# Kernel tuning notes

Measured on AMD Instinct MI355X. Metric: run time of the kernel, lower is better.

Reference implementation:

```python
import jax, jax.numpy as jnp
import numpy as np

B, N, M, C, H, NNZ = 64, 2048, 2048, 64, 128, 32768


def setup_inputs() -> dict:
    key = jax.random.key(0)
    ks = jax.random.split(key, 7)
    x = jax.random.normal(ks[0], (B * N, H), dtype=jnp.float32)
    batch = jnp.repeat(jnp.arange(B, dtype=jnp.int32), N)  # sorted graph ids
    d_rows = jax.random.randint(ks[1], (B, NNZ), 0, M, dtype=jnp.int32)
    d_cols = jax.random.randint(ks[2], (B, NNZ), 0, N, dtype=jnp.int32)
    d_vals = jax.random.normal(ks[3], (B, NNZ), dtype=jnp.float32) * (1.0 / np.sqrt(16.0))
    d_index = jax.random.randint(ks[4], (B, M), 0, C, dtype=jnp.int32)
    w_scale = 1.0 / np.sqrt(3 * H)
    Wq = jax.random.normal(ks[5], (3 * H, H), dtype=jnp.float32) * w_scale
    Wk = jax.random.normal(ks[6], (3 * H, H), dtype=jnp.float32) * w_scale
    Wv = jax.random.normal(jax.random.fold_in(key, 7), (3 * H, H), dtype=jnp.float32) * w_scale
    return {"x": x, "batch": batch, "batch_size": B, "d_rows": d_rows,
            "d_cols": d_cols, "d_vals": d_vals, "d_index": d_index,
            "Wq": Wq, "Wk": Wk, "Wv": Wv}


def _per_graph(xg, rows, cols, vals, idx, Wq, Wk, Wv):
    # spmm: coefs[r] = sum_e vals[e] * xg[cols[e]] for rows[e] == r  -> [M, H]
    coefs = jax.ops.segment_sum(vals[:, None] * xg[cols], rows, num_segments=M)
    # three segment poolings over cluster index -> each [C, H]
    s = jax.ops.segment_sum(coefs, idx, num_segments=C)
    cnt = jax.ops.segment_sum(jnp.ones((M,), coefs.dtype), idx, num_segments=C)
    mean = s / jnp.maximum(cnt, 1.0)[:, None]
    mx = jax.ops.segment_max(coefs, idx, num_segments=C)
    x_dec = jnp.concatenate([mean, mx, s], axis=1)  # [C, 3H]
    # small self-attention over clusters (linear layers without bias)
    Q = x_dec @ Wq
    K = x_dec @ Wk
    V = x_dec @ Wv
    dist = jax.nn.softmax((Q @ K.T) * (1.0 / np.sqrt(H)), axis=-1)
    return (dist @ V).reshape(-1)  # [C*H]


def reference(x, batch, batch_size, d_rows, d_cols, d_vals, d_index, Wq, Wk, Wv):
    # nodes are sorted by graph with equal graph size N, so x[batch==i] == xb[i]
    xb = x.reshape(batch_size, N, H)
    out = jax.vmap(_per_graph, in_axes=(0, 0, 0, 0, 0, None, None, None))(
        xb, d_rows, d_cols, d_vals, d_index, Wq, Wk, Wv)
    return out  # [B, C*H] == torch.vstack of per-graph flattened attentions
```

## Files before the change

### kernel.cpp

```cpp
#include <hip/hip_runtime.h>
#include <hip/hip_fp16.h>

#define BG 64
#define NN 2048
#define MM 2048
#define CC 64
#define HH 128
#define NNZE 32768
#define TH 384

typedef float f4v __attribute__((ext_vector_type(4)));
typedef __attribute__((ext_vector_type(8))) short bf16x8;
typedef __attribute__((ext_vector_type(4))) float f32x4;
typedef unsigned short u16;

static __device__ __forceinline__ u16 bf16rne(float f) {
    uint u = __float_as_uint(f);
    uint r = u + 0x7FFFu + ((u >> 16) & 1u);
    return (u16)(r >> 16);
}
static __device__ __forceinline__ float bf16tof(u16 h) {
    return __uint_as_float(((uint)h) << 16);
}

__global__ __launch_bounds__(1024) void prep_all_kernel(
    const int* __restrict__ d_rows, const int* __restrict__ d_cols,
    const float* __restrict__ d_vals, const int* __restrict__ d_index,
    const float* __restrict__ x,
    const float* __restrict__ Wq, const float* __restrict__ Wk,
    const float* __restrict__ Wv,
    uint* __restrict__ xh, u16* __restrict__ WhT, u16* __restrict__ WlT,
    int* __restrict__ cnt_clu_g, int* __restrict__ off_clu_g,
    int* __restrict__ row_edge_off_g, int2* __restrict__ epack) {
    __shared__ int cnt_row_s[MM];
    __shared__ int off_row_s[MM];
    __shared__ int fill_s[MM];
    __shared__ int rlist_s[MM];
    __shared__ int cnt_clu_s[CC], off_clu_s[CC], fill_clu_s[CC];
    __shared__ int wsum[16];
    int g = blockIdx.x, t = threadIdx.x;
    int lane = t & 63, w = t >> 6;

    cnt_row_s[t] = 0;
    cnt_row_s[t + 1024] = 0;
    fill_s[t] = 0;
    fill_s[t + 1024] = 0;
    if (t < CC) {
        cnt_clu_s[t] = 0;
        fill_clu_s[t] = 0;
    }
    int idx0 = d_index[(g << 11) + t];
    int idx1 = d_index[(g << 11) + t + 1024];
    __syncthreads();

    const int4* rows4 = (const int4*)(d_rows + ((size_t)g << 15));
#pragma unroll
    for (int it = 0; it < 8; it++) {
        int4 r = rows4[it * 1024 + t];
        atomicAdd(&cnt_row_s[r.x], 1);
        atomicAdd(&cnt_row_s[r.y], 1);
        atomicAdd(&cnt_row_s[r.z], 1);
        atomicAdd(&cnt_row_s[r.w], 1);
    }
    atomicAdd(&cnt_clu_s[idx0], 1);
    atomicAdd(&cnt_clu_s[idx1], 1);
    __syncthreads();

    if (t < CC) {
        int v = cnt_clu_s[t];
        int incl = v;
#pragma unroll
        for (int d = 1; d < 64; d <<= 1) {
            int u = __shfl_up(incl, d);
            if (t >= d) incl += u;
        }
        off_clu_s[t] = incl - v;
        cnt_clu_g[(g << 6) + t] = v;
        off_clu_g[(g << 6) + t] = incl - v;
    }
    __syncthreads();

    {
        int s0 = atomicAdd(&fill_clu_s[idx0], 1);
        rlist_s[off_clu_s[idx0] + s0] = t;
        int s1 = atomicAdd(&fill_clu_s[idx1], 1);
        rlist_s[off_clu_s[idx1] + s1] = t + 1024;
    }
    __syncthreads();

    int r0 = rlist_s[2 * t], r1 = rlist_s[2 * t + 1];
    int c0 = cnt_row_s[r0], c1 = cnt_row_s[r1];
    int s = c0 + c1;
    int incl = s;
#pragma unroll
    for (int d = 1; d < 64; d <<= 1) {
        int u = __shfl_up(incl, d);
        if (lane >= d) incl += u;
    }
    if (lane == 63) wsum[w] = incl;
    __syncthreads();
    if (t < 16) {
        int v = wsum[t], iv = v;
#pragma unroll
        for (int d = 1; d < 16; d <<= 1) {
            int u = __shfl_up(iv, d);
            if (t >= d) iv += u;
        }
        wsum[t] = iv - v;
    }
    __syncthreads();
    {
        int base = wsum[w] + incl - s;
        int* reo = row_edge_off_g + g * (MM + 1);
        reo[2 * t] = base;
        reo[2 * t + 1] = base + c0;
        off_row_s[r0] = base;
        off_row_s[r1] = base + c0;
        if (t == 0) reo[MM] = NNZE;
    }
    __syncthreads();

    const int4* cols4 = (const int4*)(d_cols + ((size_t)g << 15));
    const f4v* vals4 = (const f4v*)(d_vals + ((size_t)g << 15));
    int2* epg = epack + ((size_t)g << 15);
#pragma unroll
    for (int it = 0; it < 8; it++) {
        int4 r = rows4[it * 1024 + t];
        int4 c = cols4[it * 1024 + t];
        f4v v = vals4[it * 1024 + t];
        {
            int sl = atomicAdd(&fill_s[r.x], 1);
            int flag = (sl == cnt_row_s[r.x] - 1) ? (int)0x80000000 : 0;
            epg[off_row_s[r.x] + sl] = make_int2(c.x | flag, __float_as_int(v.x));
        }
        {
            int sl = atomicAdd(&fill_s[r.y], 1);
            int flag = (sl == cnt_row_s[r.y] - 1) ? (int)0x80000000 : 0;
            epg[off_row_s[r.y] + sl] = make_int2(c.y | flag, __float_as_int(v.y));
        }
        {
            int sl = atomicAdd(&fill_s[r.z], 1);
            int flag = (sl == cnt_row_s[r.z] - 1) ? (int)0x80000000 : 0;
            epg[off_row_s[r.z] + sl] = make_int2(c.z | flag, __float_as_int(v.z));
        }
        {
            int sl = atomicAdd(&fill_s[r.w], 1);
            int flag = (sl == cnt_row_s[r.w] - 1) ? (int)0x80000000 : 0;
            epg[off_row_s[r.w] + sl] = make_int2(c.w | flag, __float_as_int(v.w));
        }
    }

    {
        const f4v* x4 = (const f4v*)(x + ((size_t)g << 18));
        uint4* xh4 = (uint4*)(xh + ((size_t)g << 17));
#pragma unroll 4
        for (int it = 0; it < 32; it++) {
            int gi = it * 1024 + t;
            f4v a = __builtin_nontemporal_load(&x4[2 * gi]);
            f4v b = __builtin_nontemporal_load(&x4[2 * gi + 1]);
            __half2 h0 = __float22half2_rn(make_float2(a.x, a.y));
            __half2 h1 = __float22half2_rn(make_float2(a.z, a.w));
            __half2 h2 = __float22half2_rn(make_float2(b.x, b.y));
            __half2 h3 = __float22half2_rn(make_float2(b.z, b.w));
            uint4 o;
            o.x = *(uint*)&h0;
            o.y = *(uint*)&h1;
            o.z = *(uint*)&h2;
            o.w = *(uint*)&h3;
            xh4[gi] = o;
        }
    }
    for (int i = t; i < 2304; i += 1024) {
        int id = g * 2304 + i;
        int wsel = id / 49152;
        int r = id - wsel * 49152;
        const float* Ws = (wsel == 0) ? Wq : (wsel == 1) ? Wk : Wv;
        float v = Ws[r];
        int k = r >> 7, n = r & 127;
        u16 hi = bf16rne(v);
        u16 lo = bf16rne(v - bf16tof(hi));
        WhT[wsel * 49152 + n * 384 + k] = hi;
        WlT[wsel * 49152 + n * 384 + k] = lo;
    }
}

__global__ __launch_bounds__(64) void spmm_pool_kernel(const uint* __restrict__ xh,
                                                       const int* __restrict__ cnt_clu,
                                                       const int* __restrict__ off_clu,
                                                       const int* __restrict__ row_edge_off,
                                                       const int2* __restrict__ epack,
                                                       u16* __restrict__ xdh,
                                                       u16* __restrict__ xdl) {
    int bid = blockIdx.x;
    int l = bid >> 3;
    int g = ((bid & 7) << 3) + (l >> 6);
    int c = l & 63;
    int h = threadIdx.x;
    int gc = (g << 6) + c;
    int rcnt = cnt_clu[gc];
    int j0 = off_clu[gc];
    const int* reo = row_edge_off + g * (MM + 1) + j0;
    int ebase = reo[0];
    int etot = reo[rcnt] - ebase;
    const long long* ep = (const long long*)(epack + ((size_t)g << 15)) + ebase;
    const uint* xg = xh + ((size_t)g << 17);
    float2 coef = make_float2(0.f, 0.f), sum = make_float2(0.f, 0.f);
    float2 mx = make_float2(-__builtin_inff(), -__builtin_inff());
    int e = 0;
    for (; e + 16 <= etot; e += 16) {
        long long q[16];
#pragma unroll
        for (int k = 0; k < 16; k++) q[k] = __builtin_nontemporal_load(&ep[e + k]);
        uint xv[16];
#pragma unroll
        for (int k = 0; k < 16; k++)
            xv[k] = xg[(((uint)(int)q[k] & 0x7FFFFFFFu) << 6) + h];
#pragma unroll
        for (int k = 0; k < 16; k++) {
            float v = __int_as_float((int)(q[k] >> 32));
            float2 f = __half22float2(*(__half2*)&xv[k]);
            coef.x = fmaf(v, f.x, coef.x);
            coef.y = fmaf(v, f.y, coef.y);
            if ((int)q[k] < 0) {
                sum.x += coef.x; sum.y += coef.y;
                mx.x = fmaxf(mx.x, coef.x); mx.y = fmaxf(mx.y, coef.y);
                coef.x = 0.f; coef.y = 0.f;
            }
        }
    }
    for (; e < etot; e++) {
        long long q = ep[e];
        uint xv = xg[(((uint)(int)q & 0x7FFFFFFFu) << 6) + h];
        float v = __int_as_float((int)(q >> 32));
        float2 f = __half22float2(*(__half2*)&xv);
        coef.x = fmaf(v, f.x, coef.x);
        coef.y = fmaf(v, f.y, coef.y);
        if ((int)q < 0) {
            sum.x += coef.x; sum.y += coef.y;
            mx.x = fmaxf(mx.x, coef.x); mx.y = fmaxf(mx.y, coef.y);
            coef.x = 0.f; coef.y = 0.f;
        }
    }
    int az = 0;
    for (int j = h; j < rcnt; j += 64) az |= (reo[j + 1] == reo[j]);
    if (__ballot(az) != 0ULL) {
        mx.x = fmaxf(mx.x, 0.f);
        mx.y = fmaxf(mx.y, 0.f);
    }
    float inv = 1.f / (float)(rcnt > 0 ? rcnt : 1);
    uint* oh = (uint*)xdh + (size_t)gc * 192 + h;
    uint* ol = (uint*)xdl + (size_t)gc * 192 + h;
    float me0 = sum.x * inv, me1 = sum.y * inv;
    u16 a0 = bf16rne(me0), a1 = bf16rne(me1);
    oh[0] = (uint)a0 | ((uint)a1 << 16);
    ol[0] = (uint)bf16rne(me0 - bf16tof(a0)) | ((uint)bf16rne(me1 - bf16tof(a1)) << 16);
    u16 b0 = bf16rne(mx.x), b1 = bf16rne(mx.y);
    oh[64] = (uint)b0 | ((uint)b1 << 16);
    ol[64] = (uint)bf16rne(mx.x - bf16tof(b0)) | ((uint)bf16rne(mx.y - bf16tof(b1)) << 16);
    u16 c0 = bf16rne(sum.x), c1 = bf16rne(sum.y);
    oh[128] = (uint)c0 | ((uint)c1 << 16);
    ol[128] = (uint)bf16rne(sum.x - bf16tof(c0)) | ((uint)bf16rne(sum.y - bf16tof(c1)) << 16);
}

__global__ __launch_bounds__(256) void qkv_kernel(const u16* __restrict__ xdh,
                                                  const u16* __restrict__ xdl,
                                                  const u16* __restrict__ WhT,
                                                  const u16* __restrict__ WlT,
                                                  float* __restrict__ QKV) {
    __shared__ u16 Ah[64][40], Al[64][40], Bh[64][40], Bl[64][40];
    int bx = blockIdx.x, by = blockIdx.y;
    int t = threadIdx.x;
    int w = by >> 1;
    int cb = (by & 1) << 6;
    int r0 = bx << 6;
    const u16* wh = WhT + w * 49152;
    const u16* wl = WlT + w * 49152;
    int lane = t & 63, wv = t >> 6;
    int wm = wv >> 1, wn = wv & 1;
    int srow = t >> 2, sks = (t & 3) << 3;
    int fr = lane & 15, fk = (lane >> 4) << 3;
    f32x4 acc[2][2];
#pragma unroll
    for (int i = 0; i < 2; i++)
#pragma unroll
        for (int j = 0; j < 2; j++)
#pragma unroll
            for (int r = 0; r < 4; r++) acc[i][j][r] = 0.f;
    for (int ks = 0; ks < 12; ks++) {
        int k0 = ks << 5;
        bf16x8 sa_h = *(const bf16x8*)&xdh[(size_t)(r0 + srow) * 384 + k0 + sks];
        bf16x8 sa_l = *(const bf16x8*)&xdl[(size_t)(r0 + srow) * 384 + k0 + sks];
        bf16x8 sb_h = *(const bf16x8*)&wh[(size_t)(cb + srow) * 384 + k0 + sks];
        bf16x8 sb_l = *(const bf16x8*)&wl[(size_t)(cb + srow) * 384 + k0 + sks];
        if (ks) __syncthreads();
        *(bf16x8*)&Ah[srow][sks] = sa_h;
        *(bf16x8*)&Al[srow][sks] = sa_l;
        *(bf16x8*)&Bh[srow][sks] = sb_h;
        *(bf16x8*)&Bl[srow][sks] = sb_l;
        __syncthreads();
        bf16x8 fa_h[2], fa_l[2], fb_h[2], fb_l[2];
#pragma unroll
        for (int mi = 0; mi < 2; mi++) {
            int ar = (wm << 5) + (mi << 4) + fr;
            fa_h[mi] = *(const bf16x8*)&Ah[ar][fk];
            fa_l[mi] = *(const bf16x8*)&Al[ar][fk];
        }
#pragma unroll
        for (int ni = 0; ni < 2; ni++) {
            int br = (wn << 5) + (ni << 4) + fr;
            fb_h[ni] = *(const bf16x8*)&Bh[br][fk];
            fb_l[ni] = *(const bf16x8*)&Bl[br][fk];
        }
#pragma unroll
        for (int mi = 0; mi < 2; mi++)
#pragma unroll
            for (int ni = 0; ni < 2; ni++) {
                acc[mi][ni] = __builtin_amdgcn_mfma_f32_16x16x32_bf16(
                    fa_h[mi], fb_h[ni], acc[mi][ni], 0, 0, 0);
                acc[mi][ni] = __builtin_amdgcn_mfma_f32_16x16x32_bf16(
                    fa_h[mi], fb_l[ni], acc[mi][ni], 0, 0, 0);
                acc[mi][ni] = __builtin_amdgcn_mfma_f32_16x16x32_bf16(
                    fa_l[mi], fb_h[ni], acc[mi][ni], 0, 0, 0);
            }
    }
#pragma unroll
    for (int mi = 0; mi < 2; mi++)
#pragma unroll
        for (int ni = 0; ni < 2; ni++)
#pragma unroll
            for (int r = 0; r < 4; r++) {
                int row = r0 + (wm << 5) + (mi << 4) + ((lane >> 4) << 2) + r;
                int col = (by << 6) + (wn << 5) + (ni << 4) + (lane & 15);
                QKV[(size_t)row * TH + col] = acc[mi][ni][r];
            }
}

__global__ __launch_bounds__(256) void attn_kernel(const float* __restrict__ QKV,
                                                   float* __restrict__ out) {
    __shared__ float Qs[16][132];
    __shared__ float sc[16][68];
    int g = blockIdx.x;
    int q0 = blockIdx.y * 16;
    int t = threadIdx.x;
    const float* base = QKV + (size_t)(g * CC) * TH;
    for (int u = t; u < 512; u += 256) {
        int i = u >> 5, cc = u & 31;
        *(float4*)&Qs[i][cc * 4] = *(const float4*)&base[(size_t)(q0 + i) * TH + cc * 4];
    }
    __syncthreads();
    {
        int j = t & 63, iq = t >> 6;
        float a0 = 0, a1 = 0, a2 = 0, a3 = 0;
        const float* Krow = base + (size_t)j * TH + HH;
#pragma unroll 4
        for (int cc = 0; cc < 32; cc++) {
            float4 kv = *(const float4*)&Krow[cc * 4];
            float4 q0v = *(float4*)&Qs[iq][cc * 4];
            float4 q1v = *(float4*)&Qs[4 + iq][cc * 4];
            float4 q2v = *(float4*)&Qs[8 + iq][cc * 4];
            float4 q3v = *(float4*)&Qs[12 + iq][cc * 4];
            a0 += kv.x * q0v.x + kv.y * q0v.y + kv.z * q0v.z + kv.w * q0v.w;
            a1 += kv.x * q1v.x + kv.y * q1v.y + kv.z * q1v.z + kv.w * q1v.w;
            a2 += kv.x * q2v.x + kv.y * q2v.y + kv.z * q2v.z + kv.w * q2v.w;
            a3 += kv.x * q3v.x + kv.y * q3v.y + kv.z * q3v.z + kv.w * q3v.w;
        }
        const float scale = 0.08838834764831845f;
        sc[iq][j] = a0 * scale;
        sc[4 + iq][j] = a1 * scale;
        sc[8 + iq][j] = a2 * scale;
        sc[12 + iq][j] = a3 * scale;
    }
    __syncthreads();
    {
        int i = t >> 4, l = t & 15;
        float4 sv = *(float4*)&sc[i][l * 4];
        float m = fmaxf(fmaxf(sv.x, sv.y), fmaxf(sv.z, sv.w));
#pragma unroll
        for (int d = 1; d < 16; d <<= 1) m = fmaxf(m, __shfl_xor(m, d));
        float4 p;
        p.x = __expf(sv.x - m);
        p.y = __expf(sv.y - m);
        p.z = __expf(sv.z - m);
        p.w = __expf(sv.w - m);
        float s = p.x + p.y + p.z + p.w;
#pragma unroll
        for (int d = 1; d < 16; d <<= 1) s += __shfl_xor(s, d);
        float inv = 1.0f / s;
        p.x *= inv; p.y *= inv; p.z *= inv; p.w *= inv;
        *(float4*)&sc[i][l * 4] = p;
    }
    __syncthreads();
    {
        int i = t >> 4, hq = t & 15;
        const float* Vbase = base + 2 * HH;
        float acc[8] = {};
        for (int j = 0; j < 64; j++) {
            float d = sc[i][j];
            float4 v0 = *(const float4*)&Vbase[(size_t)j * TH + hq * 8];
            float4 v1 = *(const float4*)&Vbase[(size_t)j * TH + hq * 8 + 4];
            acc[0] = fmaf(d, v0.x, acc[0]);
            acc[1] = fmaf(d, v0.y, acc[1]);
            acc[2] = fmaf(d, v0.z, acc[2]);
            acc[3] = fmaf(d, v0.w, acc[3]);
            acc[4] = fmaf(d, v1.x, acc[4]);
            acc[5] = fmaf(d, v1.y, acc[5]);
            acc[6] = fmaf(d, v1.z, acc[6]);
            acc[7] = fmaf(d, v1.w, acc[7]);
        }
        float* op = out + (size_t)g * (CC * HH) + (size_t)(q0 + i) * HH + hq * 8;
        *(float4*)&op[0] = make_float4(acc[0], acc[1], acc[2], acc[3]);
        *(float4*)&op[4] = make_float4(acc[4], acc[5], acc[6], acc[7]);
    }
}

extern "C" void kernel_launch(void* const* d_in, const int* in_sizes, int n_in,
                              void* d_out, int out_size, void* d_ws, size_t ws_size,
                              hipStream_t stream) {
    const float* x = (const float*)d_in[0];
    const int* d_rows = (const int*)d_in[3];
    const int* d_cols = (const int*)d_in[4];
    const float* d_vals = (const float*)d_in[5];
    const int* d_index = (const int*)d_in[6];
    const float* Wq = (const float*)d_in[7];
    const float* Wk = (const float*)d_in[8];
    const float* Wv = (const float*)d_in[9];
    float* out = (float*)d_out;

    char* ws = (char*)d_ws;
    size_t o = 0;
    uint* xh = (uint*)(ws + o); o += (size_t)BG * NN * (HH / 2) * 4;
    int2* epack = (int2*)(ws + o); o += (size_t)BG * NNZE * 8;
    int* row_edge_off = (int*)(ws + o); o += (size_t)BG * (MM + 1) * 4;
    int* cnt_clu = (int*)(ws + o); o += (size_t)BG * CC * 4;
    int* off_clu = (int*)(ws + o); o += (size_t)BG * CC * 4;
    u16* xdh = (u16*)(ws + o); o += (size_t)BG * CC * TH * 2;
    u16* xdl = (u16*)(ws + o); o += (size_t)BG * CC * TH * 2;
    u16* WhT = (u16*)(ws + o); o += (size_t)3 * HH * TH * 2;
    u16* WlT = (u16*)(ws + o); o += (size_t)3 * HH * TH * 2;
    float* QKV = (float*)(ws + o); o += (size_t)BG * CC * TH * 4;

    prep_all_kernel<<<BG, 1024, 0, stream>>>(d_rows, d_cols, d_vals, d_index, x,
                                             Wq, Wk, Wv, xh, WhT, WlT,
                                             cnt_clu, off_clu, row_edge_off, epack);
    spmm_pool_kernel<<<BG * CC, 64, 0, stream>>>(xh, cnt_clu, off_clu, row_edge_off,
                                                 epack, xdh, xdl);
    qkv_kernel<<<dim3(64, 6), 256, 0, stream>>>(xdh, xdl, WhT, WlT, QKV);
    attn_kernel<<<dim3(BG, 4), 256, 0, stream>>>(QKV, out);
}
```

Baseline: 309.2 us.

## Split preprocessing into count and scan/bin kernels across four blocks per graph

The single 64-block preprocessing kernel becomes two kernels that each run four 1024-thread blocks per graph. The first counts per-row edges for a quarter of the edges and writes them out, along with the fp16 conversion of x and the weight split. The second combines the four partial counts, replaces the shared-memory cluster bucketing with a per-cluster wave-scan that packs count and size into one integer, and bins its quarter of edges into the CSR layout. This spreads work over far more of the GPU's compute units, which the 64-block version left mostly idle. The cost is an extra launch, a global round trip for the partial counts, and the scan being repeated in every block of a graph.

```diff
diff --git a/kernel.cpp b/kernel.cpp
--- a/kernel.cpp
+++ b/kernel.cpp
@@ -23,164 +23,185 @@
     return __uint_as_float(((uint)h) << 16);
 }
 
-__global__ __launch_bounds__(1024) void prep_all_kernel(
+__global__ __launch_bounds__(1024) void prep_count_kernel(const int* __restrict__ d_rows,
+                                                          const float* __restrict__ x,
+                                                          const float* __restrict__ Wq,
+                                                          const float* __restrict__ Wk,
+                                                          const float* __restrict__ Wv,
+                                                          int* __restrict__ cnt_blk,
+                                                          uint* __restrict__ xh,
+                                                          u16* __restrict__ WhT,
+                                                          u16* __restrict__ WlT) {
+    __shared__ int cnt_row_s[MM];
+    int gb = blockIdx.x;
+    int g = gb >> 2, b = gb & 3;
+    int t = threadIdx.x;
+    cnt_row_s[t] = 0;
+    cnt_row_s[t + 1024] = 0;
+    __syncthreads();
+    const int* rows_g = d_rows + ((size_t)g << 15) + (b << 13);
+#pragma unroll
+    for (int it = 0; it < 8; it++) atomicAdd(&cnt_row_s[rows_g[it * 1024 + t]], 1);
+
+    {
+        const f4v* x4 = (const f4v*)x;
+        uint4* xh4 = (uint4*)xh;
+#pragma unroll
+        for (int it = 0; it < 8; it++) {
+            int tidg = (gb << 13) + it * 1024 + t;
+            f4v a = __builtin_nontemporal_load(&x4[2 * tidg]);
+            f4v bb = __builtin_nontemporal_load(&x4[2 * tidg + 1]);
+            __half2 h0 = __float22half2_rn(make_float2(a.x, a.y));
+            __half2 h1 = __float22half2_rn(make_float2(a.z, a.w));
+            __half2 h2 = __float22half2_rn(make_float2(bb.x, bb.y));
+            __half2 h3 = __float22half2_rn(make_float2(bb.z, bb.w));
+            uint4 o;
+            o.x = *(uint*)&h0;
+            o.y = *(uint*)&h1;
+            o.z = *(uint*)&h2;
+            o.w = *(uint*)&h3;
+            xh4[tidg] = o;
+        }
+    }
+    if (gb < 144) {
+        int id = (gb << 10) + t;
+        int w = id / 49152;
+        int r = id - w * 49152;
+        const float* Ws = (w == 0) ? Wq : (w == 1) ? Wk : Wv;
+        float v = Ws[r];
+        int k = r >> 7, n = r & 127;
+        u16 hi = bf16rne(v);
+        u16 lo = bf16rne(v - bf16tof(hi));
+        WhT[w * 49152 + n * 384 + k] = hi;
+        WlT[w * 49152 + n * 384 + k] = lo;
+    }
+    __syncthreads();
+    int* cb = cnt_blk + (size_t)gb * MM;
+    cb[t] = cnt_row_s[t];
+    cb[t + 1024] = cnt_row_s[t + 1024];
+}
+
+__global__ __launch_bounds__(1024) void prep_scanbin_kernel(
     const int* __restrict__ d_rows, const int* __restrict__ d_cols,
     const float* __restrict__ d_vals, const int* __restrict__ d_index,
-    const float* __restrict__ x,
-    const float* __restrict__ Wq, const float* __restrict__ Wk,
-    const float* __restrict__ Wv,
-    uint* __restrict__ xh, u16* __restrict__ WhT, u16* __restrict__ WlT,
+    const int* __restrict__ cnt_blk,
     int* __restrict__ cnt_clu_g, int* __restrict__ off_clu_g,
     int* __restrict__ row_edge_off_g, int2* __restrict__ epack) {
-    __shared__ int cnt_row_s[MM];
-    __shared__ int off_row_s[MM];
+    __shared__ int base_s[MM];
+    __shared__ int end_s[MM];
     __shared__ int fill_s[MM];
-    __shared__ int rlist_s[MM];
-    __shared__ int cnt_clu_s[CC], off_clu_s[CC], fill_clu_s[CC];
-    __shared__ int wsum[16];
-    int g = blockIdx.x, t = threadIdx.x;
+    __shared__ int wcnt[16][CC];
+    __shared__ int off_pack[CC];
+    int bid = blockIdx.x;
+    int g = ((bid & 7) << 3) | ((bid >> 3) & 7);
+    int b = bid >> 6;
+    int t = threadIdx.x;
     int lane = t & 63, w = t >> 6;
 
-    cnt_row_s[t] = 0;
-    cnt_row_s[t + 1024] = 0;
     fill_s[t] = 0;
     fill_s[t + 1024] = 0;
+    const int* cb = cnt_blk + ((size_t)g << 2) * MM;
+    for (int r = t; r < MM; r += 1024) {
+        int c0 = cb[r], c1 = cb[MM + r], c2 = cb[2 * MM + r], c3 = cb[3 * MM + r];
+        base_s[r] = (b > 0 ? c0 : 0) + (b > 1 ? c1 : 0) + (b > 2 ? c2 : 0);
+        end_s[r] = c0 + c1 + c2 + c3;
+    }
+    int r0 = (w << 7) + 2 * lane;
+    int r1 = r0 + 1;
+    int idx0 = d_index[(g << 11) + r0];
+    int idx1 = d_index[(g << 11) + r1];
+    __syncthreads();
+
+    int tot0 = end_s[r0], tot1 = end_s[r1];
+    int lp0 = 0, lp1 = 0;
+    for (int c = 0; c < CC; c++) {
+        int v0 = (idx0 == c) ? (tot0 | (1 << 17)) : 0;
+        int v1 = (idx1 == c) ? (tot1 | (1 << 17)) : 0;
+        int pv = v0 + v1;
+        int incl = pv;
+#pragma unroll
+        for (int d = 1; d < 64; d <<= 1) {
+            int u = __shfl_up(incl, d);
+            if (lane >= d) incl += u;
+        }
+        int excl = incl - pv;
+        if (idx0 == c) lp0 = excl;
+        if (idx1 == c) lp1 = excl + v0;
+        if (lane == 63) wcnt[w][c] = incl;
+    }
+    __syncthreads();
     if (t < CC) {
-        cnt_clu_s[t] = 0;
-        fill_clu_s[t] = 0;
-    }
-    int idx0 = d_index[(g << 11) + t];
-    int idx1 = d_index[(g << 11) + t + 1024];
-    __syncthreads();
-
-    const int4* rows4 = (const int4*)(d_rows + ((size_t)g << 15));
-#pragma unroll
-    for (int it = 0; it < 8; it++) {
-        int4 r = rows4[it * 1024 + t];
-        atomicAdd(&cnt_row_s[r.x], 1);
-        atomicAdd(&cnt_row_s[r.y], 1);
-        atomicAdd(&cnt_row_s[r.z], 1);
-        atomicAdd(&cnt_row_s[r.w], 1);
-    }
-    atomicAdd(&cnt_clu_s[idx0], 1);
-    atomicAdd(&cnt_clu_s[idx1], 1);
-    __syncthreads();
-
-    if (t < CC) {
-        int v = cnt_clu_s[t];
-        int incl = v;
+        int tot = 0;
+#pragma unroll
+        for (int ww = 0; ww < 16; ww++) tot += wcnt[ww][t];
+        int incl = tot;
 #pragma unroll
         for (int d = 1; d < 64; d <<= 1) {
             int u = __shfl_up(incl, d);
             if (t >= d) incl += u;
         }
-        off_clu_s[t] = incl - v;
-        cnt_clu_g[(g << 6) + t] = v;
-        off_clu_g[(g << 6) + t] = incl - v;
-    }
-    __syncthreads();
-
+        off_pack[t] = incl - tot;
+        if (b == 0) {
+            cnt_clu_g[(g << 6) + t] = tot >> 17;
+            off_clu_g[(g << 6) + t] = (incl - tot) >> 17;
+        }
+    }
+    __syncthreads();
     {
-        int s0 = atomicAdd(&fill_clu_s[idx0], 1);
-        rlist_s[off_clu_s[idx0] + s0] = t;
-        int s1 = atomicAdd(&fill_clu_s[idx1], 1);
-        rlist_s[off_clu_s[idx1] + s1] = t + 1024;
-    }
-    __syncthreads();
-
-    int r0 = rlist_s[2 * t], r1 = rlist_s[2 * t + 1];
-    int c0 = cnt_row_s[r0], c1 = cnt_row_s[r1];
-    int s = c0 + c1;
-    int incl = s;
-#pragma unroll
-    for (int d = 1; d < 64; d <<= 1) {
-        int u = __shfl_up(incl, d);
-        if (lane >= d) incl += u;
-    }
-    if (lane == 63) wsum[w] = incl;
-    __syncthreads();
-    if (t < 16) {
-        int v = wsum[t], iv = v;
-#pragma unroll
-        for (int d = 1; d < 16; d <<= 1) {
-            int u = __shfl_up(iv, d);
-            if (t >= d) iv += u;
-        }
-        wsum[t] = iv - v;
-    }
-    __syncthreads();
-    {
-        int base = wsum[w] + incl - s;
-        int* reo = row_edge_off_g + g * (MM + 1);
-        reo[2 * t] = base;
-        reo[2 * t + 1] = base + c0;
-        off_row_s[r0] = base;
-        off_row_s[r1] = base + c0;
-        if (t == 0) reo[MM] = NNZE;
-    }
-    __syncthreads();
-
-    const int4* cols4 = (const int4*)(d_cols + ((size_t)g << 15));
-    const f4v* vals4 = (const f4v*)(d_vals + ((size_t)g << 15));
+        int wb0 = off_pack[idx0], wb1 = off_pack[idx1];
+        for (int ww = 0; ww < w; ww++) {
+            wb0 += wcnt[ww][idx0];
+            wb1 += wcnt[ww][idx1];
+        }
+        int p0 = wb0 + lp0, p1 = wb1 + lp1;
+        int off0 = p0 & 0x1FFFF, rk0 = p0 >> 17;
+        int off1 = p1 & 0x1FFFF, rk1 = p1 >> 17;
+        if (b == 0) {
+            int* reo = row_edge_off_g + g * (MM + 1);
+            reo[rk0] = off0;
+            reo[rk1] = off1;
+            if (t == 0) reo[MM] = NNZE;
+        }
+        base_s[r0] += off0;
+        end_s[r0] = off0 + tot0;
+        base_s[r1] += off1;
+        end_s[r1] = off1 + tot1;
+    }
+    __syncthreads();
+
+    const int4* rows4 = (const int4*)(d_rows + ((size_t)g << 15) + (b << 13));
+    const int4* cols4 = (const int4*)(d_cols + ((size_t)g << 15) + (b << 13));
+    const f4v* vals4 = (const f4v*)(d_vals + ((size_t)g << 15) + (b << 13));
     int2* epg = epack + ((size_t)g << 15);
 #pragma unroll
-    for (int it = 0; it < 8; it++) {
+    for (int it = 0; it < 2; it++) {
         int4 r = rows4[it * 1024 + t];
         int4 c = cols4[it * 1024 + t];
         f4v v = vals4[it * 1024 + t];
         {
             int sl = atomicAdd(&fill_s[r.x], 1);
-            int flag = (sl == cnt_row_s[r.x] - 1) ? (int)0x80000000 : 0;
-            epg[off_row_s[r.x] + sl] = make_int2(c.x | flag, __float_as_int(v.x));
+            int pos = base_s[r.x] + sl;
+            int flag = (pos == end_s[r.x] - 1) ? (int)0x80000000 : 0;
+            epg[pos] = make_int2(c.x | flag, __float_as_int(v.x));
         }
         {
             int sl = atomicAdd(&fill_s[r.y], 1);
-            int flag = (sl == cnt_row_s[r.y] - 1) ? (int)0x80000000 : 0;
-            epg[off_row_s[r.y] + sl] = make_int2(c.y | flag, __float_as_int(v.y));
+            int pos = base_s[r.y] + sl;
+            int flag = (pos == end_s[r.y] - 1) ? (int)0x80000000 : 0;
+            epg[pos] = make_int2(c.y | flag, __float_as_int(v.y));
         }
         {
             int sl = atomicAdd(&fill_s[r.z], 1);
-            int flag = (sl == cnt_row_s[r.z] - 1) ? (int)0x80000000 : 0;
-            epg[off_row_s[r.z] + sl] = make_int2(c.z | flag, __float_as_int(v.z));
+            int pos = base_s[r.z] + sl;
+            int flag = (pos == end_s[r.z] - 1) ? (int)0x80000000 : 0;
+            epg[pos] = make_int2(c.z | flag, __float_as_int(v.z));
         }
         {
             int sl = atomicAdd(&fill_s[r.w], 1);
-            int flag = (sl == cnt_row_s[r.w] - 1) ? (int)0x80000000 : 0;
-            epg[off_row_s[r.w] + sl] = make_int2(c.w | flag, __float_as_int(v.w));
-        }
-    }
-
-    {
-        const f4v* x4 = (const f4v*)(x + ((size_t)g << 18));
-        uint4* xh4 = (uint4*)(xh + ((size_t)g << 17));
-#pragma unroll 4
-        for (int it = 0; it < 32; it++) {
-            int gi = it * 1024 + t;
-            f4v a = __builtin_nontemporal_load(&x4[2 * gi]);
-            f4v b = __builtin_nontemporal_load(&x4[2 * gi + 1]);
-            __half2 h0 = __float22half2_rn(make_float2(a.x, a.y));
-            __half2 h1 = __float22half2_rn(make_float2(a.z, a.w));
-            __half2 h2 = __float22half2_rn(make_float2(b.x, b.y));
-            __half2 h3 = __float22half2_rn(make_float2(b.z, b.w));
-            uint4 o;
-            o.x = *(uint*)&h0;
-            o.y = *(uint*)&h1;
-            o.z = *(uint*)&h2;
-            o.w = *(uint*)&h3;
-            xh4[gi] = o;
-        }
-    }
-    for (int i = t; i < 2304; i += 1024) {
-        int id = g * 2304 + i;
-        int wsel = id / 49152;
-        int r = id - wsel * 49152;
-        const float* Ws = (wsel == 0) ? Wq : (wsel == 1) ? Wk : Wv;
-        float v = Ws[r];
-        int k = r >> 7, n = r & 127;
-        u16 hi = bf16rne(v);
-        u16 lo = bf16rne(v - bf16tof(hi));
-        WhT[wsel * 49152 + n * 384 + k] = hi;
-        WlT[wsel * 49152 + n * 384 + k] = lo;
+            int pos = base_s[r.w] + sl;
+            int flag = (pos == end_s[r.w] - 1) ? (int)0x80000000 : 0;
+            epg[pos] = make_int2(c.w | flag, __float_as_int(v.w));
+        }
     }
 }
 
@@ -430,6 +451,7 @@
     size_t o = 0;
     uint* xh = (uint*)(ws + o); o += (size_t)BG * NN * (HH / 2) * 4;
     int2* epack = (int2*)(ws + o); o += (size_t)BG * NNZE * 8;
+    int* cnt_blk = (int*)(ws + o); o += (size_t)BG * 4 * MM * 4;
     int* row_edge_off = (int*)(ws + o); o += (size_t)BG * (MM + 1) * 4;
     int* cnt_clu = (int*)(ws + o); o += (size_t)BG * CC * 4;
     int* off_clu = (int*)(ws + o); o += (size_t)BG * CC * 4;
@@ -439,9 +461,11 @@
     u16* WlT = (u16*)(ws + o); o += (size_t)3 * HH * TH * 2;
     float* QKV = (float*)(ws + o); o += (size_t)BG * CC * TH * 4;
 
-    prep_all_kernel<<<BG, 1024, 0, stream>>>(d_rows, d_cols, d_vals, d_index, x,
-                                             Wq, Wk, Wv, xh, WhT, WlT,
-                                             cnt_clu, off_clu, row_edge_off, epack);
+    prep_count_kernel<<<BG * 4, 1024, 0, stream>>>(d_rows, x, Wq, Wk, Wv,
+                                                   cnt_blk, xh, WhT, WlT);
+    prep_scanbin_kernel<<<BG * 4, 1024, 0, stream>>>(d_rows, d_cols, d_vals, d_index,
+                                                     cnt_blk,
+                                                     cnt_clu, off_clu, row_edge_off, epack);
     spmm_pool_kernel<<<BG * CC, 64, 0, stream>>>(xh, cnt_clu, off_clu, row_edge_off,
                                                  epack, xdh, xdl);
     qkv_kernel<<<dim3(64, 6), 256, 0, stream>>>(xdh, xdl, WhT, WlT, QKV);
```

After: 255.2 us. 17.5% less time.
